# Kernel tuning notes

Hardware: AMD Instinct MI355X
Metric: run time of the kernel (lower is better)

Reference implementation:

```python
import jax, jax.numpy as jnp
import numpy as np

DIM = 128
NUM_HEADS = 4
WIN = 16  # effective window: window_size(8) * sqrt(dim_t=4)
N = WIN * WIN
B_ = 512
NW = 64


def _relative_position_index(wh, ww):
    coords = np.stack(np.meshgrid(np.arange(wh), np.arange(ww), indexing='ij'))  # (2,wh,ww)
    cf = coords.reshape(2, -1)
    rel = cf[:, :, None] - cf[:, None, :]  # (2,N,N)
    rel = rel.transpose(1, 2, 0).copy()
    rel[:, :, 0] += wh - 1
    rel[:, :, 1] += ww - 1
    rel[:, :, 0] *= 2 * ww - 1
    return rel.sum(-1).astype(np.int32)  # (N,N)


def setup_inputs() -> dict:
    key = jax.random.key(0)
    ks = jax.random.split(key, 7)
    inputs = jax.random.normal(ks[0], (B_, N, DIM), dtype=jnp.float32)
    mask = jax.random.normal(ks[1], (NW, N, N), dtype=jnp.float32)
    qkv_w = jax.random.normal(ks[2], (3 * DIM, DIM), dtype=jnp.float32) * 0.02
    qkv_b = jnp.zeros((3 * DIM,), dtype=jnp.float32)
    proj_w = jax.random.normal(ks[3], (DIM, DIM), dtype=jnp.float32) * 0.02
    proj_b = jnp.zeros((DIM,), dtype=jnp.float32)
    table_sz = (2 * WIN - 1) * (2 * WIN - 1)  # 961
    bias_table = jax.random.normal(ks[4], (table_sz, NUM_HEADS), dtype=jnp.float32) * 0.02
    rel_idx = jnp.asarray(_relative_position_index(WIN, WIN))  # (N,N) int32
    return {"inputs": inputs, "mask": mask, "qkv_w": qkv_w, "qkv_b": qkv_b,
            "proj_w": proj_w, "proj_b": proj_b, "bias_table": bias_table,
            "rel_idx": rel_idx}


def reference(inputs, mask, qkv_w, qkv_b, proj_w, proj_b, bias_table, rel_idx):
    B, Nn, C = inputs.shape
    H = bias_table.shape[1]
    Dh = C // H
    scale = Dh ** -0.5
    qkv = (inputs @ qkv_w.T + qkv_b).reshape(B, Nn, 3, H, Dh)
    qkv = jnp.transpose(qkv, (2, 0, 3, 1, 4))  # (3,B,H,N,Dh)
    q, k, v = qkv[0] * scale, qkv[1], qkv[2]
    attn = jnp.einsum('bhnd,bhmd->bhnm', q, k)  # (B,H,N,N)
    rpb = jnp.transpose(bias_table[rel_idx], (2, 0, 1))  # (H,N,N)
    attn = attn + rpb[None]
    nW = mask.shape[0]
    attn = attn.reshape(B // nW, nW, H, Nn, Nn) + mask[None, :, None]
    attn = jax.nn.softmax(attn.reshape(B, H, Nn, Nn), axis=-1)
    out = jnp.einsum('bhnm,bhmd->bhnd', attn, v)
    out = jnp.transpose(out, (0, 2, 1, 3)).reshape(B, Nn, C)
    return out @ proj_w.T + proj_b
```

## Files before the change

### kernel.cpp

```cpp
#include <hip/hip_runtime.h>

typedef __bf16 bf16;
typedef __bf16 bf16x8 __attribute__((ext_vector_type(8)));
typedef __bf16 bf16x4 __attribute__((ext_vector_type(4)));
typedef float f32x4 __attribute__((ext_vector_type(4)));

static __device__ __forceinline__ f32x4 mfma16(bf16x8 a, bf16x8 b, f32x4 c) {
  return __builtin_amdgcn_mfma_f32_16x16x32_bf16(a, b, c, 0, 0, 0);
}

static __device__ __forceinline__ bf16x8 ld_bf8(const float* __restrict__ p) {
  f32x4 a = *(const f32x4*)p;
  f32x4 b = *(const f32x4*)(p + 4);
  bf16x8 r;
  r[0] = (bf16)a[0]; r[1] = (bf16)a[1]; r[2] = (bf16)a[2]; r[3] = (bf16)a[3];
  r[4] = (bf16)b[0]; r[5] = (bf16)b[1]; r[6] = (bf16)b[2]; r[7] = (bf16)b[3];
  return r;
}

__global__ void k0_prep(const float* __restrict__ mask, const float* __restrict__ bt,
                        const int* __restrict__ ri, bf16* __restrict__ mb,
                        bf16* __restrict__ rb) {
  int t = blockIdx.x * 256 + threadIdx.x;
  f32x4 m4 = *(const f32x4*)(mask + (size_t)t * 4);
  bf16x4 o;
#pragma unroll
  for (int r = 0; r < 4; ++r) o[r] = (bf16)m4[r];
  *(bf16x4*)(mb + (size_t)t * 4) = o;
  if (t < 65536) {
    int idx = ri[t];
    f32x4 v = *(const f32x4*)(bt + idx * 4);
#pragma unroll
    for (int h = 0; h < 4; ++h) rb[h * 65536 + t] = (bf16)v[h];
  }
}

__global__ void __launch_bounds__(256, 2)
k1_qkv(const float* __restrict__ x, const float* __restrict__ qw,
       const float* __restrict__ qb, bf16* __restrict__ q_s,
       bf16* __restrict__ k_s, bf16* __restrict__ vt) {
  const int tid = threadIdx.x;
  const int wv = tid >> 6, ln = tid & 15, qd = (tid >> 4) & 3;
  const int b = blockIdx.x >> 1;
  const int row0 = (blockIdx.x & 1) * 128 + (wv >> 1) * 64;
  const int cg = wv & 1;

  bf16x8 xf[4][4];
#pragma unroll
  for (int nt = 0; nt < 4; ++nt)
#pragma unroll
    for (int ks = 0; ks < 4; ++ks)
      xf[nt][ks] = ld_bf8(x + (size_t)(b * 256 + row0 + nt * 16 + ln) * 128 +
                          ks * 32 + qd * 8);

#pragma unroll
  for (int ch = 0; ch < 2; ++ch) {
    f32x4 acc[4][4];
#pragma unroll
    for (int mt = 0; mt < 4; ++mt)
#pragma unroll
      for (int nt = 0; nt < 4; ++nt) acc[mt][nt] = (f32x4){0.f, 0.f, 0.f, 0.f};
#pragma unroll
    for (int mt = 0; mt < 4; ++mt)
#pragma unroll
      for (int ks = 0; ks < 4; ++ks) {
        bf16x8 wf = ld_bf8(qw + (size_t)(ch * 128 + cg * 64 + mt * 16 + ln) * 128 +
                           ks * 32 + qd * 8);
#pragma unroll
        for (int nt = 0; nt < 4; ++nt) acc[mt][nt] = mfma16(wf, xf[nt][ks], acc[mt][nt]);
      }
    bf16* dst = ch ? k_s : q_s;
    const float scl = ch ? 1.0f : 0.17677669529663689f;
#pragma unroll
    for (int mt = 0; mt < 4; ++mt) {
      const int c0 = cg * 64 + mt * 16 + qd * 4;
      f32x4 b4 = *(const f32x4*)(qb + ch * 128 + c0);
      const int hh = c0 >> 5, d0 = c0 & 31;
#pragma unroll
      for (int nt = 0; nt < 4; ++nt) {
        const int nr = row0 + nt * 16 + ln;
        bf16x4 o;
#pragma unroll
        for (int r = 0; r < 4; ++r) o[r] = (bf16)((acc[mt][nt][r] + b4[r]) * scl);
        *(bf16x4*)(dst + (size_t)((b * 4 + hh) * 256 + nr) * 32 + d0) = o;
      }
    }
  }

  f32x4 av[4][4];
#pragma unroll
  for (int nt = 0; nt < 4; ++nt)
#pragma unroll
    for (int mt = 0; mt < 4; ++mt) av[nt][mt] = (f32x4){0.f, 0.f, 0.f, 0.f};
#pragma unroll
  for (int ks = 0; ks < 4; ++ks)
#pragma unroll
    for (int mt = 0; mt < 4; ++mt) {
      bf16x8 wf = ld_bf8(qw + (size_t)(256 + cg * 64 + mt * 16 + ln) * 128 +
                         ks * 32 + qd * 8);
#pragma unroll
      for (int nt = 0; nt < 4; ++nt) av[nt][mt] = mfma16(xf[nt][ks], wf, av[nt][mt]);
    }
#pragma unroll
  for (int nt = 0; nt < 4; ++nt)
#pragma unroll
    for (int mt = 0; mt < 4; ++mt) {
      const int c = cg * 64 + mt * 16 + ln;
      const float bb = qb[256 + c];
      const int hh = c >> 5, dd = c & 31;
      const int n0 = row0 + nt * 16 + qd * 4;
      bf16x4 o;
#pragma unroll
      for (int r = 0; r < 4; ++r) o[r] = (bf16)(av[nt][mt][r] + bb);
      *(bf16x4*)(vt + (size_t)((b * 4 + hh) * 32 + dd) * 256 + n0) = o;
    }
}

__global__ void __launch_bounds__(256, 2)
k2_attn(bf16* __restrict__ q_s, const bf16* __restrict__ k_s,
        const bf16* __restrict__ vt, const bf16* __restrict__ mb,
        const bf16* __restrict__ rb) {
  __shared__ bf16 ksm[256 * 32];
  __shared__ bf16 vsm[32 * 256];
  __shared__ bf16 psm[4 * 16 * 256];
  const int tid = threadIdx.x, wv = tid >> 6;
  const int ln = tid & 15, qd = (tid >> 4) & 3;
  const int w = blockIdx.x & 63, h = (blockIdx.x >> 6) & 3, rh = blockIdx.x >> 8;

  bf16x4 cmb[2][16];
#pragma unroll
  for (int si = 0; si < 2; ++si) {
    const int n = (rh * 8 + wv * 2 + si) * 16 + ln;
#pragma unroll
    for (int mt = 0; mt < 16; ++mt) {
      bf16x4 m4 = *(const bf16x4*)(mb + (size_t)(w * 256 + n) * 256 + mt * 16 + qd * 4);
      bf16x4 r4 = *(const bf16x4*)(rb + (size_t)h * 65536 + n * 256 + mt * 16 + qd * 4);
      bf16x4 cv;
#pragma unroll
      for (int r = 0; r < 4; ++r) cv[r] = (bf16)((float)m4[r] + (float)r4[r]);
      cmb[si][mt] = cv;
    }
  }

  for (int ib = 0; ib < 8; ++ib) {
    const int b = w + ib * 64;
    const bf16* kp = k_s + (size_t)(b * 4 + h) * 8192;
    const bf16* vp = vt + (size_t)(b * 4 + h) * 8192;
    __syncthreads();
#pragma unroll
    for (int i = 0; i < 4; ++i) {
      const int ci = i * 256 + tid;
      {
        const int r_ = ci >> 2, cb = ci & 3;
        *(bf16x8*)(ksm + r_ * 32 + ((cb ^ (r_ & 3)) * 8)) =
            *(const bf16x8*)(kp + r_ * 32 + cb * 8);
      }
      {
        const int r_ = ci >> 5, cb = ci & 31;
        *(bf16x8*)(vsm + r_ * 256 + ((cb ^ (r_ & 7)) * 8)) =
            *(const bf16x8*)(vp + r_ * 256 + cb * 8);
      }
    }
    __syncthreads();

#pragma unroll
    for (int si = 0; si < 2; ++si) {
      const int s = rh * 8 + wv * 2 + si;
      bf16x8 qf = *(const bf16x8*)(q_s + (size_t)(b * 4 + h) * 8192 +
                                   (s * 16 + ln) * 32 + qd * 8);
      f32x4 acc[16];
#pragma unroll
      for (int mt = 0; mt < 16; ++mt) acc[mt] = (f32x4){0.f, 0.f, 0.f, 0.f};
#pragma unroll
      for (int mt = 0; mt < 16; ++mt) {
        const int m = mt * 16 + ln;
        bf16x8 af = *(const bf16x8*)(ksm + m * 32 + ((qd ^ (m & 3)) * 8));
        acc[mt] = mfma16(af, qf, acc[mt]);
      }
      float sum = 0.f;
      bf16* pb = psm + wv * 4096 + ln * 256;
#pragma unroll
      for (int mt = 0; mt < 16; ++mt) {
        bf16x4 pv;
#pragma unroll
        for (int r = 0; r < 4; ++r) {
          float p = __expf(acc[mt][r] + (float)cmb[si][mt][r]);
          sum += p;
          pv[r] = (bf16)p;
        }
        *(bf16x4*)(pb + (((mt * 2 + (qd >> 1)) ^ (ln & 7)) * 8) + (qd & 1) * 4) = pv;
      }
      sum += __shfl_xor(sum, 16);
      sum += __shfl_xor(sum, 32);
      const float linv = 1.0f / sum;

      f32x4 accO[2];
      accO[0] = (f32x4){0.f, 0.f, 0.f, 0.f};
      accO[1] = (f32x4){0.f, 0.f, 0.f, 0.f};
#pragma unroll
      for (int kt = 0; kt < 8; ++kt) {
        bf16x8 pf = *(const bf16x8*)(pb + (((kt * 4 + qd) ^ (ln & 7)) * 8));
#pragma unroll
        for (int ct = 0; ct < 2; ++ct) {
          const int d = ct * 16 + ln;
          bf16x8 vf = *(const bf16x8*)(vsm + d * 256 + (((kt * 4 + qd) ^ (d & 7)) * 8));
          accO[ct] = mfma16(pf, vf, accO[ct]);
        }
      }
#pragma unroll
      for (int r = 0; r < 4; ++r) {
        const float lb = __shfl(linv, qd * 4 + r);
        const size_t obase =
            (size_t)(b * 4 + h) * 8192 + (size_t)(s * 16 + qd * 4 + r) * 32;
#pragma unroll
        for (int ct = 0; ct < 2; ++ct)
          q_s[obase + ct * 16 + ln] = (bf16)(accO[ct][r] * lb);
      }
    }
  }
}

__global__ void __launch_bounds__(256, 2)
k3_proj(const bf16* __restrict__ xb, const float* __restrict__ pw,
        const float* __restrict__ pbias, float* __restrict__ out) {
  const int tid = threadIdx.x;
  const int wv = tid >> 6, ln = tid & 15, qd = (tid >> 4) & 3;
  const int cg = wv & 1;
  const size_t row0 = (size_t)blockIdx.x * 128 + (wv >> 1) * 64;

  bf16x8 xf[4][4];
#pragma unroll
  for (int nt = 0; nt < 4; ++nt) {
    const size_t row = row0 + nt * 16 + ln;
    const size_t b = row >> 8, n = row & 255;
#pragma unroll
    for (int ks = 0; ks < 4; ++ks)
      xf[nt][ks] = *(const bf16x8*)(xb + ((b * 4 + ks) * 256 + n) * 32 + qd * 8);
  }

  f32x4 acc[4][4];
#pragma unroll
  for (int mt = 0; mt < 4; ++mt)
#pragma unroll
    for (int nt = 0; nt < 4; ++nt) acc[mt][nt] = (f32x4){0.f, 0.f, 0.f, 0.f};
#pragma unroll
  for (int mt = 0; mt < 4; ++mt)
#pragma unroll
    for (int ks = 0; ks < 4; ++ks) {
      bf16x8 wf = ld_bf8(pw + (size_t)(cg * 64 + mt * 16 + ln) * 128 + ks * 32 + qd * 8);
#pragma unroll
      for (int nt = 0; nt < 4; ++nt) acc[mt][nt] = mfma16(wf, xf[nt][ks], acc[mt][nt]);
    }
#pragma unroll
  for (int mt = 0; mt < 4; ++mt) {
    const int c0 = cg * 64 + mt * 16 + qd * 4;
    f32x4 b4 = *(const f32x4*)(pbias + c0);
#pragma unroll
    for (int nt = 0; nt < 4; ++nt) {
      f32x4 o;
#pragma unroll
      for (int r = 0; r < 4; ++r) o[r] = acc[mt][nt][r] + b4[r];
      *(f32x4*)(out + (row0 + nt * 16 + ln) * 128 + c0) = o;
    }
  }
}

extern "C" void kernel_launch(void* const* d_in, const int* in_sizes, int n_in,
                              void* d_out, int out_size, void* d_ws, size_t ws_size,
                              hipStream_t stream) {
  const float* x = (const float*)d_in[0];
  const float* mask = (const float*)d_in[1];
  const float* qkv_w = (const float*)d_in[2];
  const float* qkv_b = (const float*)d_in[3];
  const float* proj_w = (const float*)d_in[4];
  const float* proj_b = (const float*)d_in[5];
  const float* bias_table = (const float*)d_in[6];
  const int* rel_idx = (const int*)d_in[7];

  char* ws = (char*)d_ws;
  bf16* q_s = (bf16*)ws;
  bf16* k_s = (bf16*)(ws + 33554432);
  bf16* vt = (bf16*)(ws + 2ll * 33554432);
  bf16* mb = (bf16*)d_out;
  bf16* rb = (bf16*)((char*)d_out + 16777216);

  k0_prep<<<dim3(4096), dim3(256), 0, stream>>>(mask, bias_table, rel_idx, mb, rb);
  k1_qkv<<<dim3(1024), dim3(256), 0, stream>>>(x, qkv_w, qkv_b, q_s, k_s, vt);
  k2_attn<<<dim3(512), dim3(256), 0, stream>>>(q_s, k_s, vt, mb, rb);
  k3_proj<<<dim3(1024), dim3(256), 0, stream>>>(q_s, proj_w, proj_b, (float*)d_out);
}
```

Baseline: 308.9 us.

## Pre-convert weights to bf16, fuse mask/bias prep into QKV kernel, halve tiles

Adds a tiny kernel that converts qkv and proj weights to bf16 once, so the GEMM kernels load bf16 fragments directly instead of converting fp32 per block. The mask and relative-bias conversion is merged into the QKV kernel as extra blocks, removing one launch and letting that memory-bound work overlap with the GEMM blocks. QKV and projection tiles shrink from 128 to 64 rows per block, with occupancy raised to 4 blocks per CU. This doubles the block count and the number of weight re-reads, and it adds a small extra launch.

```diff
diff --git a/kernel.cpp b/kernel.cpp
--- a/kernel.cpp
+++ b/kernel.cpp
@@ -18,36 +18,63 @@
   return r;
 }
 
-__global__ void k0_prep(const float* __restrict__ mask, const float* __restrict__ bt,
-                        const int* __restrict__ ri, bf16* __restrict__ mb,
-                        bf16* __restrict__ rb) {
+__global__ void k0w(const float* __restrict__ qw, const float* __restrict__ pw,
+                    bf16* __restrict__ wb, bf16* __restrict__ pwb) {
   int t = blockIdx.x * 256 + threadIdx.x;
-  f32x4 m4 = *(const f32x4*)(mask + (size_t)t * 4);
-  bf16x4 o;
-#pragma unroll
-  for (int r = 0; r < 4; ++r) o[r] = (bf16)m4[r];
-  *(bf16x4*)(mb + (size_t)t * 4) = o;
-  if (t < 65536) {
-    int idx = ri[t];
-    f32x4 v = *(const f32x4*)(bt + idx * 4);
-#pragma unroll
-    for (int h = 0; h < 4; ++h) rb[h * 65536 + t] = (bf16)v[h];
-  }
-}
-
-__global__ void __launch_bounds__(256, 2)
-k1_qkv(const float* __restrict__ x, const float* __restrict__ qw,
-       const float* __restrict__ qb, bf16* __restrict__ q_s,
-       bf16* __restrict__ k_s, bf16* __restrict__ vt) {
+  if (t < 12288) {
+    f32x4 v = *(const f32x4*)(qw + (size_t)t * 4);
+    bf16x4 o;
+#pragma unroll
+    for (int r = 0; r < 4; ++r) o[r] = (bf16)v[r];
+    *(bf16x4*)(wb + (size_t)t * 4) = o;
+  } else {
+    int u = t - 12288;
+    f32x4 v = *(const f32x4*)(pw + (size_t)u * 4);
+    bf16x4 o;
+#pragma unroll
+    for (int r = 0; r < 4; ++r) o[r] = (bf16)v[r];
+    *(bf16x4*)(pwb + (size_t)u * 4) = o;
+  }
+}
+
+__global__ void __launch_bounds__(256, 4)
+k1f(const float* __restrict__ x, const bf16* __restrict__ wb,
+    const float* __restrict__ qb, bf16* __restrict__ q_s, bf16* __restrict__ k_s,
+    bf16* __restrict__ vt, const float* __restrict__ mask,
+    const float* __restrict__ bt, const int* __restrict__ ri,
+    bf16* __restrict__ mb, bf16* __restrict__ rb) {
+  const int bid = blockIdx.x;
   const int tid = threadIdx.x;
+  if (bid >= 2048) {
+    if (bid < 3072) {
+      const int mid = bid - 2048;
+#pragma unroll
+      for (int it = 0; it < 4; ++it) {
+        const size_t t = (size_t)mid * 1024 + it * 256 + tid;
+        f32x4 m4 = *(const f32x4*)(mask + t * 4);
+        bf16x4 o;
+#pragma unroll
+        for (int r = 0; r < 4; ++r) o[r] = (bf16)m4[r];
+        *(bf16x4*)(mb + t * 4) = o;
+      }
+    } else {
+      const int t = (bid - 3072) * 256 + tid;
+      const int idx = ri[t];
+      f32x4 v = *(const f32x4*)(bt + idx * 4);
+#pragma unroll
+      for (int h = 0; h < 4; ++h) rb[h * 65536 + t] = (bf16)v[h];
+    }
+    return;
+  }
+
+  const int b = bid & 511, qt = bid >> 9;
   const int wv = tid >> 6, ln = tid & 15, qd = (tid >> 4) & 3;
-  const int b = blockIdx.x >> 1;
-  const int row0 = (blockIdx.x & 1) * 128 + (wv >> 1) * 64;
+  const int row0 = qt * 64 + (wv >> 1) * 32;
   const int cg = wv & 1;
 
-  bf16x8 xf[4][4];
-#pragma unroll
-  for (int nt = 0; nt < 4; ++nt)
+  bf16x8 xf[2][4];
+#pragma unroll
+  for (int nt = 0; nt < 2; ++nt)
 #pragma unroll
     for (int ks = 0; ks < 4; ++ks)
       xf[nt][ks] = ld_bf8(x + (size_t)(b * 256 + row0 + nt * 16 + ln) * 128 +
@@ -55,19 +82,19 @@
 
 #pragma unroll
   for (int ch = 0; ch < 2; ++ch) {
-    f32x4 acc[4][4];
+    f32x4 acc[4][2];
 #pragma unroll
     for (int mt = 0; mt < 4; ++mt)
 #pragma unroll
-      for (int nt = 0; nt < 4; ++nt) acc[mt][nt] = (f32x4){0.f, 0.f, 0.f, 0.f};
+      for (int nt = 0; nt < 2; ++nt) acc[mt][nt] = (f32x4){0.f, 0.f, 0.f, 0.f};
 #pragma unroll
     for (int mt = 0; mt < 4; ++mt)
 #pragma unroll
       for (int ks = 0; ks < 4; ++ks) {
-        bf16x8 wf = ld_bf8(qw + (size_t)(ch * 128 + cg * 64 + mt * 16 + ln) * 128 +
-                           ks * 32 + qd * 8);
-#pragma unroll
-        for (int nt = 0; nt < 4; ++nt) acc[mt][nt] = mfma16(wf, xf[nt][ks], acc[mt][nt]);
+        bf16x8 wf = *(const bf16x8*)(wb + (size_t)(ch * 128 + cg * 64 + mt * 16 + ln) *
+                                              128 + ks * 32 + qd * 8);
+#pragma unroll
+        for (int nt = 0; nt < 2; ++nt) acc[mt][nt] = mfma16(wf, xf[nt][ks], acc[mt][nt]);
       }
     bf16* dst = ch ? k_s : q_s;
     const float scl = ch ? 1.0f : 0.17677669529663689f;
@@ -77,7 +104,7 @@
       f32x4 b4 = *(const f32x4*)(qb + ch * 128 + c0);
       const int hh = c0 >> 5, d0 = c0 & 31;
 #pragma unroll
-      for (int nt = 0; nt < 4; ++nt) {
+      for (int nt = 0; nt < 2; ++nt) {
         const int nr = row0 + nt * 16 + ln;
         bf16x4 o;
 #pragma unroll
@@ -87,22 +114,22 @@
     }
   }
 
-  f32x4 av[4][4];
-#pragma unroll
-  for (int nt = 0; nt < 4; ++nt)
+  f32x4 av[2][4];
+#pragma unroll
+  for (int nt = 0; nt < 2; ++nt)
 #pragma unroll
     for (int mt = 0; mt < 4; ++mt) av[nt][mt] = (f32x4){0.f, 0.f, 0.f, 0.f};
 #pragma unroll
   for (int ks = 0; ks < 4; ++ks)
 #pragma unroll
     for (int mt = 0; mt < 4; ++mt) {
-      bf16x8 wf = ld_bf8(qw + (size_t)(256 + cg * 64 + mt * 16 + ln) * 128 +
-                         ks * 32 + qd * 8);
-#pragma unroll
-      for (int nt = 0; nt < 4; ++nt) av[nt][mt] = mfma16(xf[nt][ks], wf, av[nt][mt]);
-    }
-#pragma unroll
-  for (int nt = 0; nt < 4; ++nt)
+      bf16x8 wf = *(const bf16x8*)(wb + (size_t)(256 + cg * 64 + mt * 16 + ln) * 128 +
+                                   ks * 32 + qd * 8);
+#pragma unroll
+      for (int nt = 0; nt < 2; ++nt) av[nt][mt] = mfma16(xf[nt][ks], wf, av[nt][mt]);
+    }
+#pragma unroll
+  for (int nt = 0; nt < 2; ++nt)
 #pragma unroll
     for (int mt = 0; mt < 4; ++mt) {
       const int c = cg * 64 + mt * 16 + ln;
@@ -220,47 +247,49 @@
   }
 }
 
-__global__ void __launch_bounds__(256, 2)
-k3_proj(const bf16* __restrict__ xb, const float* __restrict__ pw,
+__global__ void __launch_bounds__(256, 4)
+k3_proj(const bf16* __restrict__ xb, const bf16* __restrict__ pwb,
         const float* __restrict__ pbias, float* __restrict__ out) {
+  const int bid = blockIdx.x;
+  const int b = bid & 511, qt = bid >> 9;
   const int tid = threadIdx.x;
   const int wv = tid >> 6, ln = tid & 15, qd = (tid >> 4) & 3;
   const int cg = wv & 1;
-  const size_t row0 = (size_t)blockIdx.x * 128 + (wv >> 1) * 64;
-
-  bf16x8 xf[4][4];
-#pragma unroll
-  for (int nt = 0; nt < 4; ++nt) {
-    const size_t row = row0 + nt * 16 + ln;
-    const size_t b = row >> 8, n = row & 255;
+  const int row0 = qt * 64 + (wv >> 1) * 32;
+
+  bf16x8 xf[2][4];
+#pragma unroll
+  for (int nt = 0; nt < 2; ++nt) {
+    const int n = row0 + nt * 16 + ln;
 #pragma unroll
     for (int ks = 0; ks < 4; ++ks)
-      xf[nt][ks] = *(const bf16x8*)(xb + ((b * 4 + ks) * 256 + n) * 32 + qd * 8);
-  }
-
-  f32x4 acc[4][4];
+      xf[nt][ks] = *(const bf16x8*)(xb + ((size_t)(b * 4 + ks) * 256 + n) * 32 + qd * 8);
+  }
+
+  f32x4 acc[4][2];
 #pragma unroll
   for (int mt = 0; mt < 4; ++mt)
 #pragma unroll
-    for (int nt = 0; nt < 4; ++nt) acc[mt][nt] = (f32x4){0.f, 0.f, 0.f, 0.f};
+    for (int nt = 0; nt < 2; ++nt) acc[mt][nt] = (f32x4){0.f, 0.f, 0.f, 0.f};
 #pragma unroll
   for (int mt = 0; mt < 4; ++mt)
 #pragma unroll
     for (int ks = 0; ks < 4; ++ks) {
-      bf16x8 wf = ld_bf8(pw + (size_t)(cg * 64 + mt * 16 + ln) * 128 + ks * 32 + qd * 8);
-#pragma unroll
-      for (int nt = 0; nt < 4; ++nt) acc[mt][nt] = mfma16(wf, xf[nt][ks], acc[mt][nt]);
+      bf16x8 wf = *(const bf16x8*)(pwb + (size_t)(cg * 64 + mt * 16 + ln) * 128 +
+                                   ks * 32 + qd * 8);
+#pragma unroll
+      for (int nt = 0; nt < 2; ++nt) acc[mt][nt] = mfma16(wf, xf[nt][ks], acc[mt][nt]);
     }
 #pragma unroll
   for (int mt = 0; mt < 4; ++mt) {
     const int c0 = cg * 64 + mt * 16 + qd * 4;
     f32x4 b4 = *(const f32x4*)(pbias + c0);
 #pragma unroll
-    for (int nt = 0; nt < 4; ++nt) {
+    for (int nt = 0; nt < 2; ++nt) {
       f32x4 o;
 #pragma unroll
       for (int r = 0; r < 4; ++r) o[r] = acc[mt][nt][r] + b4[r];
-      *(f32x4*)(out + (row0 + nt * 16 + ln) * 128 + c0) = o;
+      *(f32x4*)(out + (size_t)(b * 256 + row0 + nt * 16 + ln) * 128 + c0) = o;
     }
   }
 }
@@ -281,11 +310,14 @@
   bf16* q_s = (bf16*)ws;
   bf16* k_s = (bf16*)(ws + 33554432);
   bf16* vt = (bf16*)(ws + 2ll * 33554432);
+  bf16* wb = (bf16*)(ws + 3ll * 33554432);
+  bf16* pwb = (bf16*)(ws + 3ll * 33554432 + 98304);
   bf16* mb = (bf16*)d_out;
   bf16* rb = (bf16*)((char*)d_out + 16777216);
 
-  k0_prep<<<dim3(4096), dim3(256), 0, stream>>>(mask, bias_table, rel_idx, mb, rb);
-  k1_qkv<<<dim3(1024), dim3(256), 0, stream>>>(x, qkv_w, qkv_b, q_s, k_s, vt);
+  k0w<<<dim3(64), dim3(256), 0, stream>>>(qkv_w, proj_w, wb, pwb);
+  k1f<<<dim3(3328), dim3(256), 0, stream>>>(x, wb, qkv_b, q_s, k_s, vt, mask,
+                                            bias_table, rel_idx, mb, rb);
   k2_attn<<<dim3(512), dim3(256), 0, stream>>>(q_s, k_s, vt, mb, rb);
-  k3_proj<<<dim3(1024), dim3(256), 0, stream>>>(q_s, proj_w, proj_b, (float*)d_out);
-}
+  k3_proj<<<dim3(2048), dim3(256), 0, stream>>>(q_s, pwb, proj_b, (float*)d_out);
+}
```

Measured after the change: 303.6 us. No clear change (-1.7%).
